# Optimization experiments

Hardware: AMD Instinct MI355X
Metric: run time of the kernel (lower is better)

Reference implementation:

```python
import jax, jax.numpy as jnp
import numpy as np

B, T, S, U, VOCAB = 32, 64, 64, 512, 65


def setup_inputs() -> dict:
    key = jax.random.key(0)
    ks = jax.random.split(key, 16)
    sd = 0.05
    return {
        "shifted_labels": jax.random.randint(ks[0], (B, T), 0, VOCAB),
        "encoder_output": jax.random.normal(ks[1], (B, S, U), jnp.float32),
        "enc_state_h": jax.random.normal(ks[2], (B, U), jnp.float32),
        "enc_state_c": jax.random.normal(ks[3], (B, U), jnp.float32),
        # decoder LSTM params (keras gate order i,f,g,o)
        "Wx": jax.random.normal(ks[4], (VOCAB, 4 * U), jnp.float32) * sd,
        "Wh": jax.random.normal(ks[5], (U, 4 * U), jnp.float32) * sd,
        "b": jnp.zeros((4 * U,), jnp.float32),
        # Bahdanau attention params
        "W1": jax.random.normal(ks[6], (U, U), jnp.float32) * sd,
        "b1": jnp.zeros((U,), jnp.float32),
        "W2": jax.random.normal(ks[7], (U, U), jnp.float32) * sd,
        "b2": jnp.zeros((U,), jnp.float32),
        "V": jax.random.normal(ks[8], (U, 1), jnp.float32) * sd,
        "bv": jnp.zeros((1,), jnp.float32),
    }


def _lstm(xz, h0, c0, Wh):
    # xz: [B, T, 4U] precomputed input projections
    def step(carry, xz_t):
        h, c = carry
        z = xz_t + h @ Wh
        i, f, g, o = jnp.split(z, 4, axis=-1)
        c = jax.nn.sigmoid(f) * c + jax.nn.sigmoid(i) * jnp.tanh(g)
        h = jax.nn.sigmoid(o) * jnp.tanh(c)
        return (h, c), h

    (_, _), hs = jax.lax.scan(step, (h0, c0), jnp.swapaxes(xz, 0, 1))
    return jnp.swapaxes(hs, 0, 1)  # [B, T, U]


def reference(shifted_labels, encoder_output, enc_state_h, enc_state_c,
              Wx, Wh, b, W1, b1, W2, b2, V, bv):
    vocab = Wx.shape[0]
    x = jax.nn.one_hot(shifted_labels, vocab, dtype=encoder_output.dtype)  # [B,T,vocab]
    xz = jnp.einsum('btv,vk->btk', x, Wx) + b                              # [B,T,4U]
    dec = _lstm(xz, enc_state_h, enc_state_c, Wh)                          # [B,T,U]
    # Bahdanau attention, vectorized over all decoder timesteps at once
    d1 = dec @ W1 + b1                # [B,T,U]
    e2 = encoder_output @ W2 + b2     # [B,S,U]  (computed once, not per step)
    score = jnp.tanh(d1[:, :, None, :] + e2[:, None, :, :]) @ V + bv  # [B,T,S,1]
    w = jax.nn.softmax(score[..., 0], axis=-1)  # softmax over encoder positions S
    return jnp.transpose(w, (0, 2, 1))          # [B,S,T] (stack axis=2 in original)
```

## Files before the change

### kernel.cpp

```cpp
#include <hip/hip_runtime.h>
#include <hip/hip_bf16.h>


#define NB 32
#define NT 64
#define NS 64
#define NU 512
#define N4U 2048
#define NV 65
#define NWG 32

typedef unsigned int u32;
typedef __bf16 bf16_t;
typedef bf16_t bf16x8 __attribute__((ext_vector_type(8)));
typedef float f32x4 __attribute__((ext_vector_type(4)));
typedef u32 u32x4 __attribute__((ext_vector_type(4)));

__device__ __forceinline__ unsigned short f2bf(float f) {
  u32 u = __builtin_bit_cast(u32, f);
  u += 0x7fffu + ((u >> 16) & 1u);
  return (unsigned short)(u >> 16);
}
__device__ __forceinline__ float bf2f(unsigned short s) {
  return __builtin_bit_cast(float, (u32)s << 16);
}
__device__ __forceinline__ u32 pk2(float a, float b) {
  return (u32)f2bf(a) | ((u32)f2bf(b) << 16);
}
__device__ __forceinline__ float sigf(float x) { return 1.0f / (1.0f + __expf(-x)); }
__device__ __forceinline__ float tanhfast(float x) {
  float e = __expf(2.0f * x);
  return 1.0f - 2.0f / (e + 1.0f);
}

__global__ __launch_bounds__(256, 1)
void lstm_kernel(const int* __restrict__ labels,
                 const float* __restrict__ h0,
                 const float* __restrict__ c0,
                 const float* __restrict__ Wx,
                 const float* __restrict__ Wh,
                 const float* __restrict__ bias,
                 u32* __restrict__ hbuf,
                 u32* __restrict__ dec_u,
                 u32* __restrict__ flags)
{
  __shared__ float z_buf[NB][65];
  __shared__ float c_lds[NB][16];
  __shared__ float wx_lds[NV][65];
  __shared__ unsigned char lab_lds[NB * NT];

  const int tid  = threadIdx.x;
  const int g    = blockIdx.x;
  const int wave = tid >> 6, lane = tid & 63;
  const int wm   = wave >> 1, wn = wave & 1;
  const int l15  = lane & 15, l4 = lane >> 4;

  for (int i = tid; i < NV * 64; i += 256) {
    int v = i >> 6, c = i & 63;
    int j = (c >> 4) * NU + g * 16 + (c & 15);
    wx_lds[v][c] = Wx[v * N4U + j] + bias[j];
  }
  for (int i = tid; i < NB * 16; i += 256) {
    int r = i >> 4, u = i & 15;
    c_lds[r][u] = c0[r * NU + g * 16 + u];
  }
  for (int i = tid; i < NB * NT; i += 256) lab_lds[i] = (unsigned char)labels[i];

  bf16x8 bfrag[16][2];
#pragma unroll
  for (int kt = 0; kt < 16; ++kt) {
#pragma unroll
    for (int nt = 0; nt < 2; ++nt) {
      int c = wn * 32 + nt * 16 + l15;
      int j = (c >> 4) * NU + g * 16 + (c & 15);
      int kb = kt * 32 + l4 * 8;
      union { unsigned short us[8]; bf16x8 v; } bu;
#pragma unroll
      for (int e = 0; e < 8; ++e) bu.us[e] = f2bf(Wh[(kb + e) * N4U + j]);
      bfrag[kt][nt] = bu.v;
    }
  }

  const int arow = wm * 16 + l15;
  u32x4 afrag[16];
#pragma unroll
  for (int kt = 0; kt < 16; ++kt) {
    const float* hp = h0 + arow * NU + kt * 32 + l4 * 8;
    u32x4 t;
    t.x = pk2(hp[0], hp[1]); t.y = pk2(hp[2], hp[3]);
    t.z = pk2(hp[4], hp[5]); t.w = pk2(hp[6], hp[7]);
    afrag[kt] = t;
  }

  const int bb = tid >> 3;
  const int u2 = (tid & 7) * 2;
  const int ci = g * 8 + (tid & 7);

  for (int s = 0; s < NT; ++s) {
    f32x4 a00 = {0.f,0.f,0.f,0.f}, a01 = a00, a10 = a00, a11 = a00;
#pragma unroll
    for (int kt = 0; kt < 16; kt += 2) {
      bf16x8 av0 = __builtin_bit_cast(bf16x8, afrag[kt]);
      bf16x8 av1 = __builtin_bit_cast(bf16x8, afrag[kt + 1]);
      a00 = __builtin_amdgcn_mfma_f32_16x16x32_bf16(av0, bfrag[kt][0],     a00, 0, 0, 0);
      a10 = __builtin_amdgcn_mfma_f32_16x16x32_bf16(av0, bfrag[kt][1],     a10, 0, 0, 0);
      a01 = __builtin_amdgcn_mfma_f32_16x16x32_bf16(av1, bfrag[kt + 1][0], a01, 0, 0, 0);
      a11 = __builtin_amdgcn_mfma_f32_16x16x32_bf16(av1, bfrag[kt + 1][1], a11, 0, 0, 0);
    }
    f32x4 acc0 = a00 + a01, acc1 = a10 + a11;

#pragma unroll
    for (int ri = 0; ri < 4; ++ri) {
      z_buf[wm * 16 + l4 * 4 + ri][wn * 32 + l15]      = acc0[ri];
      z_buf[wm * 16 + l4 * 4 + ri][wn * 32 + 16 + l15] = acc1[ri];
    }
    __syncthreads();

    int lab = lab_lds[bb * NT + s];
    float hv[2];
#pragma unroll
    for (int q = 0; q < 2; ++q) {
      int u = u2 + q;
      float zi = z_buf[bb][u]      + wx_lds[lab][u];
      float zf = z_buf[bb][16 + u] + wx_lds[lab][16 + u];
      float zg = z_buf[bb][32 + u] + wx_lds[lab][32 + u];
      float zo = z_buf[bb][48 + u] + wx_lds[lab][48 + u];
      float cc = sigf(zf) * c_lds[bb][u] + sigf(zi) * tanhfast(zg);
      c_lds[bb][u] = cc;
      hv[q] = sigf(zo) * tanhfast(cc);
    }
    u32 pkv = pk2(hv[0], hv[1]);

    if (s == NT - 1) {
      dec_u[(bb * NT + s) * 256 + ci] = pkv;
      break;
    }

    __hip_atomic_store(hbuf + (((s + 1) & 1) << 13) + bb * 256 + ci, pkv,
                       __ATOMIC_RELAXED, __HIP_MEMORY_SCOPE_AGENT);

    asm volatile("s_waitcnt vmcnt(0)" ::: "memory");
    __syncthreads();

    if (tid == 0)
      __hip_atomic_store(flags + g, (u32)(s + 1),
                         __ATOMIC_RELAXED, __HIP_MEMORY_SCOPE_AGENT);

    dec_u[(bb * NT + s) * 256 + ci] = pkv;

    {
      const u32 target = (u32)(s + 1);
      int guard = 0;
      for (;;) {
        u32 f = target;
        if (lane < NWG)
          f = __hip_atomic_load(flags + lane, __ATOMIC_RELAXED,
                                __HIP_MEMORY_SCOPE_AGENT);
        if (__all(f >= target)) break;
        if (++guard > 300000) break;
        __builtin_amdgcn_s_sleep(1);
      }
    }

    {
      const u32* ap = hbuf + (((s + 1) & 1) << 13) + arow * 256 + l4 * 4;
      asm volatile(
        "global_load_dwordx4 %0, %16, off sc0 sc1\n\t"
        "global_load_dwordx4 %1, %16, off offset:64 sc0 sc1\n\t"
        "global_load_dwordx4 %2, %16, off offset:128 sc0 sc1\n\t"
        "global_load_dwordx4 %3, %16, off offset:192 sc0 sc1\n\t"
        "global_load_dwordx4 %4, %16, off offset:256 sc0 sc1\n\t"
        "global_load_dwordx4 %5, %16, off offset:320 sc0 sc1\n\t"
        "global_load_dwordx4 %6, %16, off offset:384 sc0 sc1\n\t"
        "global_load_dwordx4 %7, %16, off offset:448 sc0 sc1\n\t"
        "global_load_dwordx4 %8, %16, off offset:512 sc0 sc1\n\t"
        "global_load_dwordx4 %9, %16, off offset:576 sc0 sc1\n\t"
        "global_load_dwordx4 %10, %16, off offset:640 sc0 sc1\n\t"
        "global_load_dwordx4 %11, %16, off offset:704 sc0 sc1\n\t"
        "global_load_dwordx4 %12, %16, off offset:768 sc0 sc1\n\t"
        "global_load_dwordx4 %13, %16, off offset:832 sc0 sc1\n\t"
        "global_load_dwordx4 %14, %16, off offset:896 sc0 sc1\n\t"
        "global_load_dwordx4 %15, %16, off offset:960 sc0 sc1\n\t"
        "s_waitcnt vmcnt(0)"
        : "=&v"(afrag[0]),  "=&v"(afrag[1]),  "=&v"(afrag[2]),  "=&v"(afrag[3]),
          "=&v"(afrag[4]),  "=&v"(afrag[5]),  "=&v"(afrag[6]),  "=&v"(afrag[7]),
          "=&v"(afrag[8]),  "=&v"(afrag[9]),  "=&v"(afrag[10]), "=&v"(afrag[11]),
          "=&v"(afrag[12]), "=&v"(afrag[13]), "=&v"(afrag[14]), "=&v"(afrag[15])
        : "v"(ap)
        : "memory");
    }
  }
}

__global__ __launch_bounds__(256, 1)
void proj_kernel(const u32* __restrict__ dec_u,
                 const float* __restrict__ enc,
                 const float* __restrict__ W1,
                 const float* __restrict__ b1,
                 const float* __restrict__ W2,
                 const float* __restrict__ b2,
                 unsigned short* __restrict__ d1_bf,
                 unsigned short* __restrict__ e2_bf)
{
  const int tid = threadIdx.x;
  const int wave = tid >> 6, lane = tid & 63;
  const int l15 = lane & 15, l4 = lane >> 4;
  const int w  = blockIdx.x * 4 + wave;
  const int rt = w >> 3, cg = w & 7;
  const bool isdec = (rt < 128);
  const int r0 = (isdec ? rt : rt - 128) * 16;
  const float* Wm  = isdec ? W1 : W2;
  const float* bv_ = isdec ? b1 : b2;
  unsigned short* outp = isdec ? d1_bf : e2_bf;

  f32x4 acc[4] = {};
  const int arow = r0 + l15;
  for (int kt = 0; kt < 16; ++kt) {
    int k0 = kt * 32 + l4 * 8;
    bf16x8 a;
    if (isdec) {
      a = __builtin_bit_cast(bf16x8,
            *reinterpret_cast<const uint4*>(dec_u + arow * 256 + (k0 >> 1)));
    } else {
      const float* ep = enc + arow * NU + k0;
      union { unsigned short us[8]; bf16x8 v; } au;
#pragma unroll
      for (int e = 0; e < 8; ++e) au.us[e] = f2bf(ep[e]);
      a = au.v;
    }
#pragma unroll
    for (int nt = 0; nt < 4; ++nt) {
      int col = cg * 64 + nt * 16 + l15;
      union { unsigned short us[8]; bf16x8 v; } bu;
#pragma unroll
      for (int e = 0; e < 8; ++e) bu.us[e] = f2bf(Wm[(k0 + e) * NU + col]);
      acc[nt] = __builtin_amdgcn_mfma_f32_16x16x32_bf16(a, bu.v, acc[nt], 0, 0, 0);
    }
  }
#pragma unroll
  for (int nt = 0; nt < 4; ++nt) {
    int col = cg * 64 + nt * 16 + l15;
    float bc = bv_[col];
#pragma unroll
    for (int ri = 0; ri < 4; ++ri) {
      int row = r0 + l4 * 4 + ri;
      outp[row * NU + col] = f2bf(acc[nt][ri] + bc);
    }
  }
}

__global__ __launch_bounds__(256, 1)
void score_kernel(const unsigned short* __restrict__ d1_bf,
                  const unsigned short* __restrict__ e2_bf,
                  const float* __restrict__ V,
                  float* __restrict__ out)
{
  const int tid = threadIdx.x;
  const int wave = tid >> 6, lane = tid & 63;
  const int p = blockIdx.x * 4 + wave;
  const int bb = p >> 6, t = p & 63;

  union { uint4 q; unsigned short us[8]; } dv;
  dv.q = *reinterpret_cast<const uint4*>(d1_bf + (bb * 64 + t) * NU + lane * 8);
  float d1f[8], Vf[8];
#pragma unroll
  for (int e = 0; e < 8; ++e) { d1f[e] = bf2f(dv.us[e]); Vf[e] = V[lane * 8 + e]; }

  float sc = 0.f;
  for (int s = 0; s < NS; ++s) {
    union { uint4 q; unsigned short us[8]; } ev;
    ev.q = *reinterpret_cast<const uint4*>(e2_bf + (bb * 64 + s) * NU + lane * 8);
    float part = 0.f;
#pragma unroll
    for (int e = 0; e < 8; ++e) part += tanhfast(d1f[e] + bf2f(ev.us[e])) * Vf[e];
#pragma unroll
    for (int o = 32; o > 0; o >>= 1) part += __shfl_xor(part, o);
    sc = (lane == s) ? part : sc;
  }
  float m = sc;
#pragma unroll
  for (int o = 32; o > 0; o >>= 1) m = fmaxf(m, __shfl_xor(m, o));
  float ex = __expf(sc - m);
  float sum = ex;
#pragma unroll
  for (int o = 32; o > 0; o >>= 1) sum += __shfl_xor(sum, o);
  out[(bb * 64 + lane) * 64 + t] = ex / sum;
}

extern "C" void kernel_launch(void* const* d_in, const int* in_sizes, int n_in,
                              void* d_out, int out_size, void* d_ws, size_t ws_size,
                              hipStream_t stream)
{
  (void)in_sizes; (void)n_in; (void)out_size;
  const int*   labels = (const int*)  d_in[0];
  const float* enc    = (const float*)d_in[1];
  const float* h0     = (const float*)d_in[2];
  const float* c0     = (const float*)d_in[3];
  const float* Wx     = (const float*)d_in[4];
  const float* Wh     = (const float*)d_in[5];
  const float* bias   = (const float*)d_in[6];
  const float* W1     = (const float*)d_in[7];
  const float* b1     = (const float*)d_in[8];
  const float* W2     = (const float*)d_in[9];
  const float* b2     = (const float*)d_in[10];
  const float* V      = (const float*)d_in[11];

  char* ws = (char*)d_ws;
  const size_t OFS_HBUF = 1024;
  const size_t OFS_DEC  = 1u << 17;
  const size_t OFS_D1   = OFS_DEC + (2u << 20);
  const size_t OFS_E2   = OFS_D1  + (2u << 20);
  if (ws_size < OFS_E2 + (2u << 20)) return;

  u32* flags = (u32*)(ws);
  u32* hbuf  = (u32*)(ws + OFS_HBUF);
  u32* dec_u = (u32*)(ws + OFS_DEC);
  unsigned short* d1_bf = (unsigned short*)(ws + OFS_D1);
  unsigned short* e2_bf = (unsigned short*)(ws + OFS_E2);
  float* out = (float*)d_out;

  hipMemsetAsync(flags, 0, 256, stream);
  lstm_kernel<<<dim3(NWG), dim3(256), 0, stream>>>(labels, h0, c0, Wx, Wh, bias,
                                                   hbuf, dec_u, flags);
  proj_kernel<<<dim3(512), dim3(256), 0, stream>>>(dec_u, enc, W1, b1, W2, b2,
                                                   d1_bf, e2_bf);
  score_kernel<<<dim3(512), dim3(256), 0, stream>>>(d1_bf, e2_bf, V, out);
}
```

Before: 388.1 us.

## Replace flag barrier with step-tagged hidden-state polling in LSTM kernel

The separate per-workgroup flag array and its memset are removed. Each hidden-state word is now stored together with its step number as one 8-byte store, so consumers poll the data directly until every tag matches, then use it. This drops the extra flag store, flag poll and follow-up data load from each recurrent step. Each wave now loads only half of the h-tile and swaps the other half with its sibling wave through LDS. Tags are not reset between calls, so stale tags left by a previous invocation could match a later step and be read early.

```diff
diff --git a/kernel.cpp b/kernel.cpp
--- a/kernel.cpp
+++ b/kernel.cpp
@@ -15,6 +15,7 @@
 typedef bf16_t bf16x8 __attribute__((ext_vector_type(8)));
 typedef float f32x4 __attribute__((ext_vector_type(4)));
 typedef u32 u32x4 __attribute__((ext_vector_type(4)));
+typedef u32 u32x2 __attribute__((ext_vector_type(2)));
 
 __device__ __forceinline__ unsigned short f2bf(float f) {
   u32 u = __builtin_bit_cast(u32, f);
@@ -40,14 +41,14 @@
                  const float* __restrict__ Wx,
                  const float* __restrict__ Wh,
                  const float* __restrict__ bias,
-                 u32* __restrict__ hbuf,
-                 u32* __restrict__ dec_u,
-                 u32* __restrict__ flags)
+                 u32* __restrict__ hbuf2,
+                 u32* __restrict__ dec_u)
 {
   __shared__ float z_buf[NB][65];
   __shared__ float c_lds[NB][16];
   __shared__ float wx_lds[NV][65];
   __shared__ unsigned char lab_lds[NB * NT];
+  __shared__ __align__(16) u32 hx[2][2][64][36];
 
   const int tid  = threadIdx.x;
   const int g    = blockIdx.x;
@@ -130,64 +131,73 @@
       hv[q] = sigf(zo) * tanhfast(cc);
     }
     u32 pkv = pk2(hv[0], hv[1]);
-
-    if (s == NT - 1) {
-      dec_u[(bb * NT + s) * 256 + ci] = pkv;
-      break;
-    }
-
-    __hip_atomic_store(hbuf + (((s + 1) & 1) << 13) + bb * 256 + ci, pkv,
-                       __ATOMIC_RELAXED, __HIP_MEMORY_SCOPE_AGENT);
-
-    asm volatile("s_waitcnt vmcnt(0)" ::: "memory");
-    __syncthreads();
-
-    if (tid == 0)
-      __hip_atomic_store(flags + g, (u32)(s + 1),
-                         __ATOMIC_RELAXED, __HIP_MEMORY_SCOPE_AGENT);
-
     dec_u[(bb * NT + s) * 256 + ci] = pkv;
 
+    if (s == NT - 1) break;
+
     {
-      const u32 target = (u32)(s + 1);
+      u32x2 v2; v2.x = pkv; v2.y = (u32)(s + 1);
+      u32* sp = hbuf2 + (((s + 1) & 1) << 14) + bb * 512 + ci * 2;
+      asm volatile("global_store_dwordx2 %0, %1, off sc0 sc1"
+                   :: "v"(sp), "v"(v2) : "memory");
+    }
+
+    u32x4 t[16];
+    {
+      const u32* qp = hbuf2 + (((s + 1) & 1) << 14) + arow * 512
+                      + wn * 256 + l4 * 8;
+      const u32 tg = (u32)(s + 1);
       int guard = 0;
       for (;;) {
-        u32 f = target;
-        if (lane < NWG)
-          f = __hip_atomic_load(flags + lane, __ATOMIC_RELAXED,
-                                __HIP_MEMORY_SCOPE_AGENT);
-        if (__all(f >= target)) break;
-        if (++guard > 300000) break;
+        asm volatile(
+          "global_load_dwordx4 %0, %16, off sc0 sc1\n\t"
+          "global_load_dwordx4 %1, %16, off offset:16 sc0 sc1\n\t"
+          "global_load_dwordx4 %2, %16, off offset:128 sc0 sc1\n\t"
+          "global_load_dwordx4 %3, %16, off offset:144 sc0 sc1\n\t"
+          "global_load_dwordx4 %4, %16, off offset:256 sc0 sc1\n\t"
+          "global_load_dwordx4 %5, %16, off offset:272 sc0 sc1\n\t"
+          "global_load_dwordx4 %6, %16, off offset:384 sc0 sc1\n\t"
+          "global_load_dwordx4 %7, %16, off offset:400 sc0 sc1\n\t"
+          "global_load_dwordx4 %8, %16, off offset:512 sc0 sc1\n\t"
+          "global_load_dwordx4 %9, %16, off offset:528 sc0 sc1\n\t"
+          "global_load_dwordx4 %10, %16, off offset:640 sc0 sc1\n\t"
+          "global_load_dwordx4 %11, %16, off offset:656 sc0 sc1\n\t"
+          "global_load_dwordx4 %12, %16, off offset:768 sc0 sc1\n\t"
+          "global_load_dwordx4 %13, %16, off offset:784 sc0 sc1\n\t"
+          "global_load_dwordx4 %14, %16, off offset:896 sc0 sc1\n\t"
+          "global_load_dwordx4 %15, %16, off offset:912 sc0 sc1\n\t"
+          "s_waitcnt vmcnt(0)"
+          : "=&v"(t[0]),  "=&v"(t[1]),  "=&v"(t[2]),  "=&v"(t[3]),
+            "=&v"(t[4]),  "=&v"(t[5]),  "=&v"(t[6]),  "=&v"(t[7]),
+            "=&v"(t[8]),  "=&v"(t[9]),  "=&v"(t[10]), "=&v"(t[11]),
+            "=&v"(t[12]), "=&v"(t[13]), "=&v"(t[14]), "=&v"(t[15])
+          : "v"(qp)
+          : "memory");
+        bool ok = true;
+#pragma unroll
+        for (int i = 0; i < 16; ++i)
+          ok = ok && (t[i].y == tg) && (t[i].w == tg);
+        if (__all(ok)) break;
+        if (++guard > 100000) break;
         __builtin_amdgcn_s_sleep(1);
       }
     }
 
     {
-      const u32* ap = hbuf + (((s + 1) & 1) << 13) + arow * 256 + l4 * 4;
-      asm volatile(
-        "global_load_dwordx4 %0, %16, off sc0 sc1\n\t"
-        "global_load_dwordx4 %1, %16, off offset:64 sc0 sc1\n\t"
-        "global_load_dwordx4 %2, %16, off offset:128 sc0 sc1\n\t"
-        "global_load_dwordx4 %3, %16, off offset:192 sc0 sc1\n\t"
-        "global_load_dwordx4 %4, %16, off offset:256 sc0 sc1\n\t"
-        "global_load_dwordx4 %5, %16, off offset:320 sc0 sc1\n\t"
-        "global_load_dwordx4 %6, %16, off offset:384 sc0 sc1\n\t"
-        "global_load_dwordx4 %7, %16, off offset:448 sc0 sc1\n\t"
-        "global_load_dwordx4 %8, %16, off offset:512 sc0 sc1\n\t"
-        "global_load_dwordx4 %9, %16, off offset:576 sc0 sc1\n\t"
-        "global_load_dwordx4 %10, %16, off offset:640 sc0 sc1\n\t"
-        "global_load_dwordx4 %11, %16, off offset:704 sc0 sc1\n\t"
-        "global_load_dwordx4 %12, %16, off offset:768 sc0 sc1\n\t"
-        "global_load_dwordx4 %13, %16, off offset:832 sc0 sc1\n\t"
-        "global_load_dwordx4 %14, %16, off offset:896 sc0 sc1\n\t"
-        "global_load_dwordx4 %15, %16, off offset:960 sc0 sc1\n\t"
-        "s_waitcnt vmcnt(0)"
-        : "=&v"(afrag[0]),  "=&v"(afrag[1]),  "=&v"(afrag[2]),  "=&v"(afrag[3]),
-          "=&v"(afrag[4]),  "=&v"(afrag[5]),  "=&v"(afrag[6]),  "=&v"(afrag[7]),
-          "=&v"(afrag[8]),  "=&v"(afrag[9]),  "=&v"(afrag[10]), "=&v"(afrag[11]),
-          "=&v"(afrag[12]), "=&v"(afrag[13]), "=&v"(afrag[14]), "=&v"(afrag[15])
-        : "v"(ap)
-        : "memory");
+      u32* hw = &hx[wm][wn][lane][0];
+#pragma unroll
+      for (int j = 0; j < 8; ++j) {
+        u32x4 d; d.x = t[2*j].x; d.y = t[2*j].z; d.z = t[2*j+1].x; d.w = t[2*j+1].z;
+        *reinterpret_cast<u32x4*>(hw + j * 4) = d;
+        if (wn == 0) afrag[j] = d; else afrag[8 + j] = d;
+      }
+      __syncthreads();
+      const u32* hr = &hx[wm][wn ^ 1][lane][0];
+#pragma unroll
+      for (int j = 0; j < 8; ++j) {
+        u32x4 d = *reinterpret_cast<const u32x4*>(hr + j * 4);
+        if (wn == 0) afrag[8 + j] = d; else afrag[j] = d;
+      }
     }
   }
 }
@@ -306,22 +316,20 @@
   const float* V      = (const float*)d_in[11];
 
   char* ws = (char*)d_ws;
-  const size_t OFS_HBUF = 1024;
-  const size_t OFS_DEC  = 1u << 17;
-  const size_t OFS_D1   = OFS_DEC + (2u << 20);
-  const size_t OFS_E2   = OFS_D1  + (2u << 20);
+  const size_t OFS_HB2 = 1024;
+  const size_t OFS_DEC = OFS_HB2 + (1u << 18);
+  const size_t OFS_D1  = OFS_DEC + (2u << 20);
+  const size_t OFS_E2  = OFS_D1  + (2u << 20);
   if (ws_size < OFS_E2 + (2u << 20)) return;
 
-  u32* flags = (u32*)(ws);
-  u32* hbuf  = (u32*)(ws + OFS_HBUF);
+  u32* hbuf2 = (u32*)(ws + OFS_HB2);
   u32* dec_u = (u32*)(ws + OFS_DEC);
   unsigned short* d1_bf = (unsigned short*)(ws + OFS_D1);
   unsigned short* e2_bf = (unsigned short*)(ws + OFS_E2);
   float* out = (float*)d_out;
 
-  hipMemsetAsync(flags, 0, 256, stream);
   lstm_kernel<<<dim3(NWG), dim3(256), 0, stream>>>(labels, h0, c0, Wx, Wh, bias,
-                                                   hbuf, dec_u, flags);
+                                                   hbuf2, dec_u);
   proj_kernel<<<dim3(512), dim3(256), 0, stream>>>(dec_u, enc, W1, b1, W2, b2,
                                                    d1_bf, e2_bf);
   score_kernel<<<dim3(512), dim3(256), 0, stream>>>(d1_bf, e2_bf, V, out);
```

After: 440.2 us. 13.4% more time.

## Compute encoder projection in extra idle workgroups of the LSTM kernel

Applied to the files above, without the earlier changes.

Moves the encoder_output @ W2 projection out of the projection kernel and into 32 extra workgroups launched with the sequential LSTM kernel. Those workgroups run on otherwise idle CUs while the 32 LSTM workgroups step through the recurrence, so the projection overlaps with the latency-bound LSTM. The projection kernel now only handles the decoder W1 projection with half the grid. This relies on the extra workgroups not disturbing the LSTM's cross-workgroup flag synchronization or its co-residency.

```diff
diff --git a/kernel.cpp b/kernel.cpp
--- a/kernel.cpp
+++ b/kernel.cpp
@@ -40,9 +40,13 @@
                  const float* __restrict__ Wx,
                  const float* __restrict__ Wh,
                  const float* __restrict__ bias,
+                 const float* __restrict__ enc,
+                 const float* __restrict__ W2,
+                 const float* __restrict__ b2,
                  u32* __restrict__ hbuf,
                  u32* __restrict__ dec_u,
-                 u32* __restrict__ flags)
+                 u32* __restrict__ flags,
+                 unsigned short* __restrict__ e2_bf)
 {
   __shared__ float z_buf[NB][65];
   __shared__ float c_lds[NB][16];
@@ -52,8 +56,47 @@
   const int tid  = threadIdx.x;
   const int g    = blockIdx.x;
   const int wave = tid >> 6, lane = tid & 63;
-  const int wm   = wave >> 1, wn = wave & 1;
   const int l15  = lane & 15, l4 = lane >> 4;
+
+  if (g >= NWG) {
+    const int r0 = (g - NWG) * 64 + wave * 16;
+    const int arowE = r0 + l15;
+    u32x4 afragE[16];
+#pragma unroll
+    for (int kt = 0; kt < 16; ++kt) {
+      const float* ep = enc + arowE * NU + kt * 32 + l4 * 8;
+      u32x4 t;
+      t.x = pk2(ep[0], ep[1]); t.y = pk2(ep[2], ep[3]);
+      t.z = pk2(ep[4], ep[5]); t.w = pk2(ep[6], ep[7]);
+      afragE[kt] = t;
+    }
+    for (int cg = 0; cg < 8; ++cg) {
+      f32x4 acc[4] = {};
+      for (int kt = 0; kt < 16; ++kt) {
+        bf16x8 a = __builtin_bit_cast(bf16x8, afragE[kt]);
+        int k0 = kt * 32 + l4 * 8;
+#pragma unroll
+        for (int nt = 0; nt < 4; ++nt) {
+          int col = cg * 64 + nt * 16 + l15;
+          union { unsigned short us[8]; bf16x8 v; } bu;
+#pragma unroll
+          for (int e = 0; e < 8; ++e) bu.us[e] = f2bf(W2[(k0 + e) * NU + col]);
+          acc[nt] = __builtin_amdgcn_mfma_f32_16x16x32_bf16(a, bu.v, acc[nt], 0, 0, 0);
+        }
+      }
+#pragma unroll
+      for (int nt = 0; nt < 4; ++nt) {
+        int col = cg * 64 + nt * 16 + l15;
+        float bc = b2[col];
+#pragma unroll
+        for (int ri = 0; ri < 4; ++ri)
+          e2_bf[(r0 + l4 * 4 + ri) * NU + col] = f2bf(acc[nt][ri] + bc);
+      }
+    }
+    return;
+  }
+
+  const int wm = wave >> 1, wn = wave & 1;
 
   for (int i = tid; i < NV * 64; i += 256) {
     int v = i >> 6, c = i & 63;
@@ -194,57 +237,40 @@
 
 __global__ __launch_bounds__(256, 1)
 void proj_kernel(const u32* __restrict__ dec_u,
-                 const float* __restrict__ enc,
                  const float* __restrict__ W1,
                  const float* __restrict__ b1,
-                 const float* __restrict__ W2,
-                 const float* __restrict__ b2,
-                 unsigned short* __restrict__ d1_bf,
-                 unsigned short* __restrict__ e2_bf)
+                 unsigned short* __restrict__ d1_bf)
 {
   const int tid = threadIdx.x;
   const int wave = tid >> 6, lane = tid & 63;
   const int l15 = lane & 15, l4 = lane >> 4;
   const int w  = blockIdx.x * 4 + wave;
   const int rt = w >> 3, cg = w & 7;
-  const bool isdec = (rt < 128);
-  const int r0 = (isdec ? rt : rt - 128) * 16;
-  const float* Wm  = isdec ? W1 : W2;
-  const float* bv_ = isdec ? b1 : b2;
-  unsigned short* outp = isdec ? d1_bf : e2_bf;
+  const int r0 = rt * 16;
 
   f32x4 acc[4] = {};
   const int arow = r0 + l15;
   for (int kt = 0; kt < 16; ++kt) {
     int k0 = kt * 32 + l4 * 8;
-    bf16x8 a;
-    if (isdec) {
-      a = __builtin_bit_cast(bf16x8,
-            *reinterpret_cast<const uint4*>(dec_u + arow * 256 + (k0 >> 1)));
-    } else {
-      const float* ep = enc + arow * NU + k0;
-      union { unsigned short us[8]; bf16x8 v; } au;
-#pragma unroll
-      for (int e = 0; e < 8; ++e) au.us[e] = f2bf(ep[e]);
-      a = au.v;
-    }
+    bf16x8 a = __builtin_bit_cast(bf16x8,
+          *reinterpret_cast<const uint4*>(dec_u + arow * 256 + (k0 >> 1)));
 #pragma unroll
     for (int nt = 0; nt < 4; ++nt) {
       int col = cg * 64 + nt * 16 + l15;
       union { unsigned short us[8]; bf16x8 v; } bu;
 #pragma unroll
-      for (int e = 0; e < 8; ++e) bu.us[e] = f2bf(Wm[(k0 + e) * NU + col]);
+      for (int e = 0; e < 8; ++e) bu.us[e] = f2bf(W1[(k0 + e) * NU + col]);
       acc[nt] = __builtin_amdgcn_mfma_f32_16x16x32_bf16(a, bu.v, acc[nt], 0, 0, 0);
     }
   }
 #pragma unroll
   for (int nt = 0; nt < 4; ++nt) {
     int col = cg * 64 + nt * 16 + l15;
-    float bc = bv_[col];
+    float bc = b1[col];
 #pragma unroll
     for (int ri = 0; ri < 4; ++ri) {
       int row = r0 + l4 * 4 + ri;
-      outp[row * NU + col] = f2bf(acc[nt][ri] + bc);
+      d1_bf[row * NU + col] = f2bf(acc[nt][ri] + bc);
     }
   }
 }
@@ -320,9 +346,9 @@
   float* out = (float*)d_out;
 
   hipMemsetAsync(flags, 0, 256, stream);
-  lstm_kernel<<<dim3(NWG), dim3(256), 0, stream>>>(labels, h0, c0, Wx, Wh, bias,
-                                                   hbuf, dec_u, flags);
-  proj_kernel<<<dim3(512), dim3(256), 0, stream>>>(dec_u, enc, W1, b1, W2, b2,
-                                                   d1_bf, e2_bf);
+  lstm_kernel<<<dim3(64), dim3(256), 0, stream>>>(labels, h0, c0, Wx, Wh, bias,
+                                                  enc, W2, b2,
+                                                  hbuf, dec_u, flags, e2_bf);
+  proj_kernel<<<dim3(256), dim3(256), 0, stream>>>(dec_u, W1, b1, d1_bf);
   score_kernel<<<dim3(512), dim3(256), 0, stream>>>(d1_bf, e2_bf, V, out);
 }
```

Result: no change. 384.1 us (-1.0%).
